# Performance work log

Measured on AMD Instinct MI355X. Metric: run time of the kernel, lower is better.

## Reference

```python
import jax, jax.numpy as jnp
import numpy as np

T_MAX = 0.5
LN_EPS = 1e-5
B, N, D = 256, 16384, 512
NNZ = N * 33  # ~ (2*top_k+1) nonzeros per row of the sparse Laplacian
DF = 4 * D
DT = 32  # time-embedding hidden size


def _layernorm(x, g, b):
    mu = jnp.mean(x, axis=-1, keepdims=True)
    var = jnp.mean((x - mu) ** 2, axis=-1, keepdims=True)
    return (x - mu) * jax.lax.rsqrt(var + LN_EPS) * g + b


def setup_inputs() -> dict:
    key = jax.random.key(0)
    ks = jax.random.split(key, 16)

    def lin_w(k, fan_out, fan_in):
        return jax.random.normal(k, (fan_out, fan_in), jnp.float32) * (1.0 / np.sqrt(fan_in))

    inp = {}
    inp["x0"] = jax.random.uniform(ks[0], (B, N), jnp.float32)
    inp["t"] = jax.random.uniform(ks[1], (B,), jnp.float32)
    inp["L_vals"] = jax.random.normal(ks[2], (NNZ,), jnp.float32) * 0.1
    inp["W_in"] = lin_w(ks[3], D, N)
    inp["b_in"] = jnp.zeros((D,), jnp.float32)
    inp["W_out"] = lin_w(ks[4], N, D)
    inp["b_out"] = jnp.zeros((N,), jnp.float32)
    inp["W_qkv"] = lin_w(ks[5], 3 * D, D)
    inp["b_qkv"] = jnp.zeros((3 * D,), jnp.float32)
    inp["W_o"] = lin_w(ks[6], D, D)
    inp["b_o"] = jnp.zeros((D,), jnp.float32)
    inp["g1"] = jnp.ones((D,), jnp.float32)
    inp["be1"] = jnp.zeros((D,), jnp.float32)
    inp["g2"] = jnp.ones((D,), jnp.float32)
    inp["be2"] = jnp.zeros((D,), jnp.float32)
    inp["W_f1"] = lin_w(ks[7], DF, D)
    inp["b_f1"] = jnp.zeros((DF,), jnp.float32)
    inp["W_f2"] = lin_w(ks[8], D, DF)
    inp["b_f2"] = jnp.zeros((D,), jnp.float32)
    inp["W_t1"] = lin_w(ks[9], DT, 1)
    inp["b_t1"] = jnp.zeros((DT,), jnp.float32)
    inp["W_t2"] = lin_w(ks[10], D, DT)
    inp["b_t2"] = jnp.zeros((D,), jnp.float32)
    inp["L_rows"] = jax.random.randint(ks[11], (NNZ,), 0, N, jnp.int32)
    inp["L_cols"] = jax.random.randint(ks[12], (NNZ,), 0, N, jnp.int32)
    return inp


def reference(x0, t, L_vals, W_in, b_in, W_out, b_out, W_qkv, b_qkv, W_o, b_o,
              g1, be1, g2, be2, W_f1, b_f1, W_f2, b_f2, W_t1, b_t1, W_t2, b_t2,
              L_rows, L_cols):
    n_items = x0.shape[1]
    d_model = W_in.shape[0]
    t_cont = t * T_MAX  # per-sample diffusion time (explicit input, not RNG)

    # Batched sparse Laplacian diffusion (replaces the per-row torch.sparse.mm loop):
    # (L @ x.T)[i, b] = sum_e L_vals[e] * x0[b, L_cols[e]] aggregated to row L_rows[e]
    contrib = x0[:, L_cols] * L_vals                                  # (B, NNZ)
    Lx = jax.ops.segment_sum(contrib.T, L_rows, num_segments=n_items)  # (N, B)
    x_t = x0 - t_cont[:, None] * Lx.T                                  # (B, N)

    # Denoiser (eval mode: dropout off)
    h = x_t @ W_in.T + b_in                                            # (B, D)
    t_norm = t_cont / T_MAX
    te = jax.nn.silu(t_norm[:, None] @ W_t1.T + b_t1) @ W_t2.T + b_t2  # (B, D)
    h = h + te

    # MultiheadAttention on a length-1 sequence: softmax over one key is exactly 1,
    # so attn_out = out_proj(V) with V = h @ W_v.T + b_v.
    qkv = h @ W_qkv.T + b_qkv                                          # (B, 3D)
    v = qkv[:, 2 * d_model:]
    attn_out = v @ W_o.T + b_o

    h = _layernorm(h + attn_out, g1, be1)
    ff = jax.nn.gelu(h @ W_f1.T + b_f1, approximate=False) @ W_f2.T + b_f2
    h = _layernorm(h + ff, g2, be2)

    pred = h @ W_out.T + b_out                                         # (B, N)
    return jnp.mean((pred - x0) ** 2)
```

## Files before the change

kernel.cpp:

```cpp
#include <hip/hip_runtime.h>
#include <math.h>

#define Bb   256
#define Nn   16384
#define Dd   512
#define NNZn 540672
#define DFf  2048
#define SLOT 128

typedef __bf16 bf16;
typedef __bf16 bf16x4 __attribute__((ext_vector_type(4)));
typedef __bf16 bf16x8 __attribute__((ext_vector_type(8)));
typedef float  f32x4  __attribute__((ext_vector_type(4)));

__device__ __forceinline__ void gload16(const void* g, void* l) {
  __builtin_amdgcn_global_load_lds(
      (const __attribute__((address_space(1))) unsigned int*)g,
      (__attribute__((address_space(3))) unsigned int*)l, 16, 0, 0);
}

__global__ __launch_bounds__(256) void k_cvt_all(
    const float* __restrict__ w_in, const float* __restrict__ w_out,
    const float* __restrict__ w_v, const float* __restrict__ w_o,
    const float* __restrict__ w_f1, const float* __restrict__ w_f2,
    bf16* __restrict__ o_in, bf16* __restrict__ o_out, bf16* __restrict__ o_v,
    bf16* __restrict__ o_o, bf16* __restrict__ o_f1, bf16* __restrict__ o_f2) {
  int v = blockIdx.x * 256 + threadIdx.x;
  const float* s; bf16* d; int base;
  if (v < 4194304) {
    if (v < 2097152) { s = w_in;  d = o_in;  base = 0; }
    else             { s = w_out; d = o_out; base = 2097152; }
  } else if (v < 4325376) {
    if (v < 4259840) { s = w_v;   d = o_v;   base = 4194304; }
    else             { s = w_o;   d = o_o;   base = 4259840; }
  } else {
    if (v < 4587520) { s = w_f1;  d = o_f1;  base = 4325376; }
    else             { s = w_f2;  d = o_f2;  base = 4587520; }
  }
  int idx = (v - base) * 4;
  float4 x = *(const float4*)(s + idx);
  bf16x4 o;
  o[0] = (bf16)x.x; o[1] = (bf16)x.y; o[2] = (bf16)x.z; o[3] = (bf16)x.w;
  *(bf16x4*)(d + idx) = o;
}

__global__ __launch_bounds__(256) void k_transpose(const float* __restrict__ x0,
                                                   bf16* __restrict__ x0T) {
  __shared__ float tile[64][65];
  int n0 = blockIdx.x * 64, b0 = blockIdx.y * 64;
  int tx = threadIdx.x & 63, ty = threadIdx.x >> 6;
#pragma unroll
  for (int i = 0; i < 16; i++) {
    int bl = ty * 16 + i;
    tile[bl][tx] = x0[(size_t)(b0 + bl) * Nn + n0 + tx];
  }
  __syncthreads();
#pragma unroll
  for (int i = 0; i < 16; i++) {
    int nl = ty * 16 + i;
    x0T[(size_t)(n0 + nl) * Bb + b0 + tx] = (bf16)tile[tx][nl];
  }
}

__global__ __launch_bounds__(256) void k_bucket(const int* __restrict__ rows,
                                                const int* __restrict__ cols,
                                                const float* __restrict__ vals,
                                                int* __restrict__ counts,
                                                int* __restrict__ cols_p,
                                                float* __restrict__ vals_p) {
  int i = blockIdx.x * 256 + threadIdx.x;
  int r = rows[i];
  int p = atomicAdd(&counts[r], 1);
  if (p < SLOT) {
    cols_p[(size_t)r * SLOT + p] = cols[i];
    vals_p[(size_t)r * SLOT + p] = vals[i];
  }
}

__global__ __launch_bounds__(256) void k_lx(const bf16x4* __restrict__ x0T4,
                                            const int* __restrict__ counts,
                                            const int* __restrict__ cols_p,
                                            const float* __restrict__ vals_p,
                                            bf16x4* __restrict__ Lx4) {
  int w = threadIdx.x >> 6, lane = threadIdx.x & 63;
  int r = blockIdx.x * 4 + w;
  __shared__ int   csm[4][64];
  __shared__ float vsm[4][64];
  int cnt = counts[r];
  const int*   cp = cols_p + (size_t)r * SLOT;
  const float* vp = vals_p + (size_t)r * SLOT;
  float a0 = 0.f, a1 = 0.f, a2 = 0.f, a3 = 0.f;
  float b0 = 0.f, b1 = 0.f, b2 = 0.f, b3 = 0.f;
  for (int base = 0; base < cnt; base += 64) {
    int m = cnt - base; if (m > 64) m = 64;
    if (lane < m) { csm[w][lane] = cp[base + lane]; vsm[w][lane] = vp[base + lane]; }
    int i = 0;
    for (; i + 1 < m; i += 2) {
      bf16x4 xv0 = x0T4[(size_t)csm[w][i]     * 64 + lane];
      bf16x4 xv1 = x0T4[(size_t)csm[w][i + 1] * 64 + lane];
      float v0 = vsm[w][i], v1 = vsm[w][i + 1];
      a0 += v0 * (float)xv0[0]; a1 += v0 * (float)xv0[1];
      a2 += v0 * (float)xv0[2]; a3 += v0 * (float)xv0[3];
      b0 += v1 * (float)xv1[0]; b1 += v1 * (float)xv1[1];
      b2 += v1 * (float)xv1[2]; b3 += v1 * (float)xv1[3];
    }
    if (i < m) {
      bf16x4 xv0 = x0T4[(size_t)csm[w][i] * 64 + lane];
      float v0 = vsm[w][i];
      a0 += v0 * (float)xv0[0]; a1 += v0 * (float)xv0[1];
      a2 += v0 * (float)xv0[2]; a3 += v0 * (float)xv0[3];
    }
  }
  bf16x4 o;
  o[0] = (bf16)(a0 + b0); o[1] = (bf16)(a1 + b1);
  o[2] = (bf16)(a2 + b2); o[3] = (bf16)(a3 + b3);
  Lx4[(size_t)r * 64 + lane] = o;
}

__global__ __launch_bounds__(256) void k_combine(const float* __restrict__ x0,
                                                 const bf16* __restrict__ Lx,
                                                 const float* __restrict__ t,
                                                 bf16* __restrict__ xt) {
  __shared__ float lxs[64][65];
  int n0 = blockIdx.x * 64, b0 = blockIdx.y * 64;
  int tx = threadIdx.x & 63, ty = threadIdx.x >> 6;
#pragma unroll
  for (int i = 0; i < 16; i++) {
    int nl = ty * 16 + i;
    lxs[nl][tx] = (float)Lx[(size_t)(n0 + nl) * Bb + b0 + tx];
  }
  __syncthreads();
#pragma unroll
  for (int i = 0; i < 16; i++) {
    int bl = ty * 16 + i;
    int b  = b0 + bl;
    float tc = t[b] * 0.5f;
    float v = x0[(size_t)b * Nn + n0 + tx] - tc * lxs[tx][bl];
    xt[(size_t)b * Nn + n0 + tx] = (bf16)v;
  }
}

template <int BM, int BN, int MODE, int ACT = 0>
__global__ __launch_bounds__(256) void gemm_tn(
    const bf16* __restrict__ A, const bf16* __restrict__ Bm,
    float* __restrict__ C, int N, int K, int kLen, int MN,
    const float* __restrict__ bias, const float* __restrict__ x0,
    float* __restrict__ lossOut) {
  constexpr int WM = BM / 2, WN = BN / 2, FM = WM / 16, FN = WN / 16;
  constexpr int PA = (BM * 64) / 4096, PB = (BN * 64) / 4096;
  __shared__ __align__(16) bf16 As[BM * 32];
  __shared__ __align__(16) bf16 Bs[BN * 32];
  const int tid = threadIdx.x;
  const int lane = tid & 63, w = tid >> 6;
  const int wm = w >> 1, wn = w & 1;
  const int mBase = blockIdx.x * BM, nBase = blockIdx.y * BN;
  const int k0 = blockIdx.z * kLen;

  f32x4 acc[FM][FN];
#pragma unroll
  for (int i = 0; i < FM; i++)
#pragma unroll
    for (int j = 0; j < FN; j++) acc[i][j] = {0.f, 0.f, 0.f, 0.f};

  for (int kk = 0; kk < kLen; kk += 32) {
    const int k = k0 + kk;
    __syncthreads();
#pragma unroll
    for (int p = 0; p < PA; p++) {
      int u = p * 256 + tid;
      gload16(A + (size_t)(mBase + (u >> 2)) * K + k + (u & 3) * 8,
              (char*)As + p * 4096 + w * 1024);
    }
#pragma unroll
    for (int p = 0; p < PB; p++) {
      int u = p * 256 + tid;
      gload16(Bm + (size_t)(nBase + (u >> 2)) * K + k + (u & 3) * 8,
              (char*)Bs + p * 4096 + w * 1024);
    }
    __syncthreads();
    bf16x8 af[FM], bfr[FN];
#pragma unroll
    for (int i = 0; i < FM; i++)
      af[i] = *(const bf16x8*)(As + (wm * WM + i * 16 + (lane & 15)) * 32 + (lane >> 4) * 8);
#pragma unroll
    for (int j = 0; j < FN; j++)
      bfr[j] = *(const bf16x8*)(Bs + (wn * WN + j * 16 + (lane & 15)) * 32 + (lane >> 4) * 8);
#pragma unroll
    for (int i = 0; i < FM; i++)
#pragma unroll
      for (int j = 0; j < FN; j++)
        acc[i][j] = __builtin_amdgcn_mfma_f32_16x16x32_bf16(af[i], bfr[j], acc[i][j], 0, 0, 0);
  }

  if constexpr (MODE == 0) {
    float* Cz = C + (size_t)blockIdx.z * MN;
#pragma unroll
    for (int i = 0; i < FM; i++)
#pragma unroll
      for (int j = 0; j < FN; j++) {
        int n  = nBase + wn * WN + j * 16 + (lane & 15);
        int mB = mBase + wm * WM + i * 16 + ((lane >> 4) << 2);
#pragma unroll
        for (int r = 0; r < 4; r++)
          Cz[(size_t)(mB + r) * N + n] = acc[i][j][r];
      }
  } else if constexpr (MODE == 1) {
    bf16* Cb = (bf16*)C;
#pragma unroll
    for (int i = 0; i < FM; i++)
#pragma unroll
      for (int j = 0; j < FN; j++) {
        int n  = nBase + wn * WN + j * 16 + (lane & 15);
        float bo = bias[n];
        int mB = mBase + wm * WM + i * 16 + ((lane >> 4) << 2);
#pragma unroll
        for (int r = 0; r < 4; r++) {
          float x = acc[i][j][r] + bo;
          if constexpr (ACT == 1)
            x = 0.5f * x * (1.f + erff(x * 0.70710678118654752f));
          Cb[(size_t)(mB + r) * N + n] = (bf16)x;
        }
      }
  } else {
    float lsum = 0.f;
#pragma unroll
    for (int i = 0; i < FM; i++)
#pragma unroll
      for (int j = 0; j < FN; j++) {
        int n  = nBase + wn * WN + j * 16 + (lane & 15);
        float bo = bias[n];
        int mB = mBase + wm * WM + i * 16 + ((lane >> 4) << 2);
#pragma unroll
        for (int r = 0; r < 4; r++) {
          float d = acc[i][j][r] + bo - x0[(size_t)(mB + r) * N + n];
          lsum += d * d;
        }
      }
    for (int off = 32; off > 0; off >>= 1) lsum += __shfl_down(lsum, off, 64);
    if (lane == 0) atomicAdd(lossOut, lsum);
  }
}

__global__ __launch_bounds__(512) void k_epi_h(const float* __restrict__ P,
                                               const float* __restrict__ t,
                                               const float* __restrict__ W_t1,
                                               const float* __restrict__ b_t1,
                                               const float* __restrict__ W_t2,
                                               const float* __restrict__ b_t2,
                                               const float* __restrict__ b_in,
                                               float* __restrict__ h_f32,
                                               bf16* __restrict__ h_b) {
  int b = blockIdx.x, d = threadIdx.x;
  __shared__ float s[32];
  if (d < 32) {
    float z = t[b] * W_t1[d] + b_t1[d];
    s[d] = z / (1.f + expf(-z));
  }
  __syncthreads();
  int i = b * Dd + d;
  float v = b_in[d] + b_t2[d];
#pragma unroll
  for (int sp = 0; sp < 32; sp++) v += P[sp * (Bb * Dd) + i];
#pragma unroll
  for (int j = 0; j < 32; j++) v += s[j] * W_t2[d * 32 + j];
  h_f32[i] = v;
  h_b[i] = (bf16)v;
}

template <int NS>
__global__ __launch_bounds__(512) void k_ln(const float* __restrict__ base,
                                            const float* __restrict__ add,
                                            const float* __restrict__ bias,
                                            const float* __restrict__ g,
                                            const float* __restrict__ be,
                                            float* __restrict__ out_f32,
                                            bf16* __restrict__ out_b) {
  int b = blockIdx.x, d = threadIdx.x;
  __shared__ float red[16];
  int i = b * Dd + d;
  float x = base[i] + bias[d];
#pragma unroll
  for (int sp = 0; sp < NS; sp++) x += add[sp * (Bb * Dd) + i];
  int w = d >> 6, lane = d & 63;
  float s = x;
  for (int off = 32; off > 0; off >>= 1) s += __shfl_down(s, off, 64);
  if (lane == 0) red[w] = s;
  __syncthreads();
  if (d == 0) {
    float tot = 0.f;
    for (int q = 0; q < 8; q++) tot += red[q];
    red[8] = tot * (1.f / 512.f);
  }
  __syncthreads();
  float mu = red[8];
  float c = x - mu;
  float s2 = c * c;
  for (int off = 32; off > 0; off >>= 1) s2 += __shfl_down(s2, off, 64);
  if (lane == 0) red[w] = s2;
  __syncthreads();
  if (d == 0) {
    float tot = 0.f;
    for (int q = 0; q < 8; q++) tot += red[q];
    red[8] = tot * (1.f / 512.f);
  }
  __syncthreads();
  float var = red[8];
  float y = c * rsqrtf(var + 1e-5f) * g[d] + be[d];
  if (out_f32) out_f32[i] = y;
  out_b[i] = (bf16)y;
}

__global__ void k_final(const float* __restrict__ loss, float* __restrict__ out) {
  if (threadIdx.x == 0 && blockIdx.x == 0)
    out[0] = loss[0] * (1.f / 4194304.f);
}

extern "C" void kernel_launch(void* const* d_in, const int* in_sizes, int n_in,
                              void* d_out, int out_size, void* d_ws, size_t ws_size,
                              hipStream_t stream) {
  const float* x0    = (const float*)d_in[0];
  const float* t     = (const float*)d_in[1];
  const float* Lv    = (const float*)d_in[2];
  const float* W_in  = (const float*)d_in[3];
  const float* b_in  = (const float*)d_in[4];
  const float* W_out = (const float*)d_in[5];
  const float* b_out = (const float*)d_in[6];
  const float* W_qkv = (const float*)d_in[7];
  const float* b_qkv = (const float*)d_in[8];
  const float* W_o   = (const float*)d_in[9];
  const float* b_o   = (const float*)d_in[10];
  const float* g1    = (const float*)d_in[11];
  const float* be1   = (const float*)d_in[12];
  const float* g2    = (const float*)d_in[13];
  const float* be2   = (const float*)d_in[14];
  const float* W_f1  = (const float*)d_in[15];
  const float* b_f1  = (const float*)d_in[16];
  const float* W_f2  = (const float*)d_in[17];
  const float* b_f2  = (const float*)d_in[18];
  const float* W_t1  = (const float*)d_in[19];
  const float* b_t1  = (const float*)d_in[20];
  const float* W_t2  = (const float*)d_in[21];
  const float* b_t2  = (const float*)d_in[22];
  const int* L_rows  = (const int*)d_in[23];
  const int* L_cols  = (const int*)d_in[24];

  size_t off = 0;
  char* ws = (char*)d_ws;
  auto carve = [&](size_t bytes) -> void* {
    void* p = ws + off;
    off += (bytes + 255) & ~(size_t)255;
    return p;
  };

  bf16* W_in_b   = (bf16*)carve((size_t)Dd * Nn * 2);
  bf16* W_out_b  = (bf16*)carve((size_t)Nn * Dd * 2);
  bf16* W_v_b    = (bf16*)carve((size_t)Dd * Dd * 2);
  bf16* W_o_b    = (bf16*)carve((size_t)Dd * Dd * 2);
  bf16* W_f1_b   = (bf16*)carve((size_t)DFf * Dd * 2);
  bf16* W_f2_b   = (bf16*)carve((size_t)Dd * DFf * 2);
  bf16* x0T_b    = (bf16*)carve((size_t)Nn * Bb * 2);
  bf16* Lx_b     = (bf16*)carve((size_t)Nn * Bb * 2);
  bf16* xt_b     = (bf16*)carve((size_t)Bb * Nn * 2);
  float* p_h     = (float*)carve((size_t)32 * Bb * Dd * 4);
  float* p_at    = (float*)carve((size_t)Bb * Dd * 4);
  float* p_f2    = (float*)carve((size_t)4 * Bb * Dd * 4);
  float* h_f32   = (float*)carve((size_t)Bb * Dd * 4);
  bf16* h_b      = (bf16*)carve((size_t)Bb * Dd * 2);
  bf16* v_b      = (bf16*)carve((size_t)Bb * Dd * 2);
  float* hln_f32 = (float*)carve((size_t)Bb * Dd * 4);
  bf16* hln_b    = (bf16*)carve((size_t)Bb * Dd * 2);
  bf16* f1_b     = (bf16*)carve((size_t)Bb * DFf * 2);
  bf16* h2_b     = (bf16*)carve((size_t)Bb * Dd * 2);
  int* counts    = (int*)carve((size_t)Nn * 4);
  float* lossw   = (float*)carve(256);
  int* cols_p    = (int*)carve((size_t)Nn * SLOT * 4);
  float* vals_p  = (float*)carve((size_t)Nn * SLOT * 4);
  (void)in_sizes; (void)n_in; (void)out_size; (void)ws_size;

  hipMemsetAsync(counts, 0, (size_t)Nn * 4 + 256, stream);

  k_cvt_all<<<18944, 256, 0, stream>>>(
      W_in, W_out, W_qkv + (size_t)2 * Dd * Dd, W_o, W_f1, W_f2,
      W_in_b, W_out_b, W_v_b, W_o_b, W_f1_b, W_f2_b);

  k_transpose<<<dim3(256, 4), 256, 0, stream>>>(x0, x0T_b);
  k_bucket<<<NNZn / 256, 256, 0, stream>>>(L_rows, L_cols, Lv, counts, cols_p, vals_p);
  k_lx<<<Nn / 4, 256, 0, stream>>>((const bf16x4*)x0T_b, counts, cols_p, vals_p,
                                   (bf16x4*)Lx_b);
  k_combine<<<dim3(256, 4), 256, 0, stream>>>(x0, Lx_b, t, xt_b);

  gemm_tn<128, 128, 0><<<dim3(2, 4, 32), 256, 0, stream>>>(
      xt_b, W_in_b, p_h, Dd, Nn, 512, Bb * Dd, nullptr, nullptr, nullptr);
  k_epi_h<<<Bb, 512, 0, stream>>>(p_h, t, W_t1, b_t1, W_t2, b_t2, b_in, h_f32, h_b);

  gemm_tn<64, 64, 1><<<dim3(4, 8, 1), 256, 0, stream>>>(
      h_b, W_v_b, (float*)v_b, Dd, Dd, 512, 0, b_qkv + 2 * Dd, nullptr, nullptr);

  gemm_tn<64, 64, 0><<<dim3(4, 8, 1), 256, 0, stream>>>(
      v_b, W_o_b, p_at, Dd, Dd, 512, 0, nullptr, nullptr, nullptr);
  k_ln<1><<<Bb, 512, 0, stream>>>(h_f32, p_at, b_o, g1, be1, hln_f32, hln_b);

  gemm_tn<64, 64, 1, 1><<<dim3(4, 32, 1), 256, 0, stream>>>(
      hln_b, W_f1_b, (float*)f1_b, DFf, Dd, 512, 0, b_f1, nullptr, nullptr);

  gemm_tn<64, 64, 0><<<dim3(4, 8, 4), 256, 0, stream>>>(
      f1_b, W_f2_b, p_f2, Dd, DFf, 512, Bb * Dd, nullptr, nullptr, nullptr);
  k_ln<4><<<Bb, 512, 0, stream>>>(hln_f32, p_f2, b_f2, g2, be2, nullptr, h2_b);

  gemm_tn<128, 128, 2><<<dim3(2, 128, 1), 256, 0, stream>>>(
      h2_b, W_out_b, nullptr, Nn, Dd, 512, 0, b_out, x0, lossw);
  k_final<<<1, 64, 0, stream>>>(lossw, (float*)d_out);
}
```

Before: 338.2 us.

## Fuse prep kernels, pack sparse entries, convert large weights inside GEMM loads

Merges the weight conversion, x0 transpose and COO bucketing into one launch. It drops the separate fp32-to-bf16 passes for the two large N×D weights (W_in, W_out); their GEMMs now read fp32 B tiles and convert them while storing to shared memory. Sparse column and value pairs are stored together as int2, so k_lx does one load per entry instead of two. This removes a large conversion write and read plus two launches. The trade is that those GEMMs move twice the B bytes and use synchronous register-staged loads instead of direct global-to-LDS loads.

New measurement: 329.6 us. -2.5%, faster.

```diff
diff --git a/kernel.cpp b/kernel.cpp
--- a/kernel.cpp
+++ b/kernel.cpp
@@ -8,6 +8,10 @@
 #define DFf  2048
 #define SLOT 128
 
+#define CVT_BLKS 2560
+#define TR_BLKS  1024
+#define BK_BLKS  2112
+
 typedef __bf16 bf16;
 typedef __bf16 bf16x4 __attribute__((ext_vector_type(4)));
 typedef __bf16 bf16x8 __attribute__((ext_vector_type(8)));
@@ -19,94 +23,85 @@
       (__attribute__((address_space(3))) unsigned int*)l, 16, 0, 0);
 }
 
-__global__ __launch_bounds__(256) void k_cvt_all(
-    const float* __restrict__ w_in, const float* __restrict__ w_out,
+__global__ __launch_bounds__(256) void k_prep(
     const float* __restrict__ w_v, const float* __restrict__ w_o,
     const float* __restrict__ w_f1, const float* __restrict__ w_f2,
-    bf16* __restrict__ o_in, bf16* __restrict__ o_out, bf16* __restrict__ o_v,
-    bf16* __restrict__ o_o, bf16* __restrict__ o_f1, bf16* __restrict__ o_f2) {
-  int v = blockIdx.x * 256 + threadIdx.x;
-  const float* s; bf16* d; int base;
-  if (v < 4194304) {
-    if (v < 2097152) { s = w_in;  d = o_in;  base = 0; }
-    else             { s = w_out; d = o_out; base = 2097152; }
-  } else if (v < 4325376) {
-    if (v < 4259840) { s = w_v;   d = o_v;   base = 4194304; }
-    else             { s = w_o;   d = o_o;   base = 4259840; }
+    bf16* __restrict__ o_v, bf16* __restrict__ o_o,
+    bf16* __restrict__ o_f1, bf16* __restrict__ o_f2,
+    const float* __restrict__ x0, bf16* __restrict__ x0T,
+    const int* __restrict__ rows, const int* __restrict__ cols,
+    const float* __restrict__ vals,
+    int* __restrict__ counts, int2* __restrict__ ents) {
+  __shared__ float tile[64][65];
+  int blk = blockIdx.x;
+  if (blk < CVT_BLKS) {
+    int v = blk * 256 + threadIdx.x;
+    const float* s; bf16* d; int base;
+    if (v < 131072) {
+      if (v < 65536) { s = w_v;  d = o_v;  base = 0; }
+      else           { s = w_o;  d = o_o;  base = 65536; }
+    } else {
+      if (v < 393216) { s = w_f1; d = o_f1; base = 131072; }
+      else            { s = w_f2; d = o_f2; base = 393216; }
+    }
+    int idx = (v - base) * 4;
+    float4 x = *(const float4*)(s + idx);
+    bf16x4 o;
+    o[0] = (bf16)x.x; o[1] = (bf16)x.y; o[2] = (bf16)x.z; o[3] = (bf16)x.w;
+    *(bf16x4*)(d + idx) = o;
+  } else if (blk < CVT_BLKS + TR_BLKS) {
+    int bx = blk - CVT_BLKS;
+    int n0 = (bx & 255) * 64, b0 = (bx >> 8) * 64;
+    int tx = threadIdx.x & 63, ty = threadIdx.x >> 6;
+#pragma unroll
+    for (int i = 0; i < 16; i++) {
+      int bl = ty * 16 + i;
+      tile[bl][tx] = x0[(size_t)(b0 + bl) * Nn + n0 + tx];
+    }
+    __syncthreads();
+#pragma unroll
+    for (int i = 0; i < 16; i++) {
+      int nl = ty * 16 + i;
+      x0T[(size_t)(n0 + nl) * Bb + b0 + tx] = (bf16)tile[tx][nl];
+    }
   } else {
-    if (v < 4587520) { s = w_f1;  d = o_f1;  base = 4325376; }
-    else             { s = w_f2;  d = o_f2;  base = 4587520; }
-  }
-  int idx = (v - base) * 4;
-  float4 x = *(const float4*)(s + idx);
-  bf16x4 o;
-  o[0] = (bf16)x.x; o[1] = (bf16)x.y; o[2] = (bf16)x.z; o[3] = (bf16)x.w;
-  *(bf16x4*)(d + idx) = o;
-}
-
-__global__ __launch_bounds__(256) void k_transpose(const float* __restrict__ x0,
-                                                   bf16* __restrict__ x0T) {
-  __shared__ float tile[64][65];
-  int n0 = blockIdx.x * 64, b0 = blockIdx.y * 64;
-  int tx = threadIdx.x & 63, ty = threadIdx.x >> 6;
-#pragma unroll
-  for (int i = 0; i < 16; i++) {
-    int bl = ty * 16 + i;
-    tile[bl][tx] = x0[(size_t)(b0 + bl) * Nn + n0 + tx];
-  }
-  __syncthreads();
-#pragma unroll
-  for (int i = 0; i < 16; i++) {
-    int nl = ty * 16 + i;
-    x0T[(size_t)(n0 + nl) * Bb + b0 + tx] = (bf16)tile[tx][nl];
-  }
-}
-
-__global__ __launch_bounds__(256) void k_bucket(const int* __restrict__ rows,
-                                                const int* __restrict__ cols,
-                                                const float* __restrict__ vals,
-                                                int* __restrict__ counts,
-                                                int* __restrict__ cols_p,
-                                                float* __restrict__ vals_p) {
-  int i = blockIdx.x * 256 + threadIdx.x;
-  int r = rows[i];
-  int p = atomicAdd(&counts[r], 1);
-  if (p < SLOT) {
-    cols_p[(size_t)r * SLOT + p] = cols[i];
-    vals_p[(size_t)r * SLOT + p] = vals[i];
+    int i = (blk - CVT_BLKS - TR_BLKS) * 256 + threadIdx.x;
+    int r = rows[i];
+    int p = atomicAdd(&counts[r], 1);
+    if (p < SLOT)
+      ents[(size_t)r * SLOT + p] = make_int2(cols[i], __float_as_int(vals[i]));
   }
 }
 
 __global__ __launch_bounds__(256) void k_lx(const bf16x4* __restrict__ x0T4,
                                             const int* __restrict__ counts,
-                                            const int* __restrict__ cols_p,
-                                            const float* __restrict__ vals_p,
+                                            const int2* __restrict__ ents,
                                             bf16x4* __restrict__ Lx4) {
   int w = threadIdx.x >> 6, lane = threadIdx.x & 63;
   int r = blockIdx.x * 4 + w;
-  __shared__ int   csm[4][64];
-  __shared__ float vsm[4][64];
+  __shared__ int2 esm[4][64];
   int cnt = counts[r];
-  const int*   cp = cols_p + (size_t)r * SLOT;
-  const float* vp = vals_p + (size_t)r * SLOT;
+  const int2* ep = ents + (size_t)r * SLOT;
   float a0 = 0.f, a1 = 0.f, a2 = 0.f, a3 = 0.f;
   float b0 = 0.f, b1 = 0.f, b2 = 0.f, b3 = 0.f;
   for (int base = 0; base < cnt; base += 64) {
     int m = cnt - base; if (m > 64) m = 64;
-    if (lane < m) { csm[w][lane] = cp[base + lane]; vsm[w][lane] = vp[base + lane]; }
+    if (lane < m) esm[w][lane] = ep[base + lane];
     int i = 0;
     for (; i + 1 < m; i += 2) {
-      bf16x4 xv0 = x0T4[(size_t)csm[w][i]     * 64 + lane];
-      bf16x4 xv1 = x0T4[(size_t)csm[w][i + 1] * 64 + lane];
-      float v0 = vsm[w][i], v1 = vsm[w][i + 1];
+      int2 e0 = esm[w][i], e1 = esm[w][i + 1];
+      bf16x4 xv0 = x0T4[(size_t)e0.x * 64 + lane];
+      bf16x4 xv1 = x0T4[(size_t)e1.x * 64 + lane];
+      float v0 = __int_as_float(e0.y), v1 = __int_as_float(e1.y);
       a0 += v0 * (float)xv0[0]; a1 += v0 * (float)xv0[1];
       a2 += v0 * (float)xv0[2]; a3 += v0 * (float)xv0[3];
       b0 += v1 * (float)xv1[0]; b1 += v1 * (float)xv1[1];
       b2 += v1 * (float)xv1[2]; b3 += v1 * (float)xv1[3];
     }
     if (i < m) {
-      bf16x4 xv0 = x0T4[(size_t)csm[w][i] * 64 + lane];
-      float v0 = vsm[w][i];
+      int2 e0 = esm[w][i];
+      bf16x4 xv0 = x0T4[(size_t)e0.x * 64 + lane];
+      float v0 = __int_as_float(e0.y);
       a0 += v0 * (float)xv0[0]; a1 += v0 * (float)xv0[1];
       a2 += v0 * (float)xv0[2]; a3 += v0 * (float)xv0[3];
     }
@@ -140,9 +135,9 @@
   }
 }
 
-template <int BM, int BN, int MODE, int ACT = 0>
+template <int BM, int BN, int MODE, int ACT = 0, int BF32 = 0>
 __global__ __launch_bounds__(256) void gemm_tn(
-    const bf16* __restrict__ A, const bf16* __restrict__ Bm,
+    const bf16* __restrict__ A, const void* __restrict__ Bmv,
     float* __restrict__ C, int N, int K, int kLen, int MN,
     const float* __restrict__ bias, const float* __restrict__ x0,
     float* __restrict__ lossOut) {
@@ -171,11 +166,25 @@
       gload16(A + (size_t)(mBase + (u >> 2)) * K + k + (u & 3) * 8,
               (char*)As + p * 4096 + w * 1024);
     }
-#pragma unroll
-    for (int p = 0; p < PB; p++) {
-      int u = p * 256 + tid;
-      gload16(Bm + (size_t)(nBase + (u >> 2)) * K + k + (u & 3) * 8,
-              (char*)Bs + p * 4096 + w * 1024);
+    if constexpr (BF32) {
+      const float* Bf = (const float*)Bmv;
+#pragma unroll
+      for (int p = 0; p < BN * 32 / 1024; p++) {
+        int u = p * 256 + tid;
+        int row = u >> 3, sub = u & 7;
+        float4 x = *(const float4*)(Bf + (size_t)(nBase + row) * K + k + sub * 4);
+        bf16x4 o;
+        o[0] = (bf16)x.x; o[1] = (bf16)x.y; o[2] = (bf16)x.z; o[3] = (bf16)x.w;
+        *(bf16x4*)(Bs + row * 32 + sub * 4) = o;
+      }
+    } else {
+      const bf16* Bm = (const bf16*)Bmv;
+#pragma unroll
+      for (int p = 0; p < PB; p++) {
+        int u = p * 256 + tid;
+        gload16(Bm + (size_t)(nBase + (u >> 2)) * K + k + (u & 3) * 8,
+                (char*)Bs + p * 4096 + w * 1024);
+      }
     }
     __syncthreads();
     bf16x8 af[FM], bfr[FN];
@@ -352,8 +361,6 @@
     return p;
   };
 
-  bf16* W_in_b   = (bf16*)carve((size_t)Dd * Nn * 2);
-  bf16* W_out_b  = (bf16*)carve((size_t)Nn * Dd * 2);
   bf16* W_v_b    = (bf16*)carve((size_t)Dd * Dd * 2);
   bf16* W_o_b    = (bf16*)carve((size_t)Dd * Dd * 2);
   bf16* W_f1_b   = (bf16*)carve((size_t)DFf * Dd * 2);
@@ -373,24 +380,22 @@
   bf16* h2_b     = (bf16*)carve((size_t)Bb * Dd * 2);
   int* counts    = (int*)carve((size_t)Nn * 4);
   float* lossw   = (float*)carve(256);
-  int* cols_p    = (int*)carve((size_t)Nn * SLOT * 4);
-  float* vals_p  = (float*)carve((size_t)Nn * SLOT * 4);
-  (void)in_sizes; (void)n_in; (void)out_size; (void)ws_size;
+  int2* ents     = (int2*)carve((size_t)Nn * SLOT * 8);
+  (void)in_sizes; (void)n_in; (void)out_size; (void)ws_size; (void)Lv;
 
   hipMemsetAsync(counts, 0, (size_t)Nn * 4 + 256, stream);
 
-  k_cvt_all<<<18944, 256, 0, stream>>>(
-      W_in, W_out, W_qkv + (size_t)2 * Dd * Dd, W_o, W_f1, W_f2,
-      W_in_b, W_out_b, W_v_b, W_o_b, W_f1_b, W_f2_b);
-
-  k_transpose<<<dim3(256, 4), 256, 0, stream>>>(x0, x0T_b);
-  k_bucket<<<NNZn / 256, 256, 0, stream>>>(L_rows, L_cols, Lv, counts, cols_p, vals_p);
-  k_lx<<<Nn / 4, 256, 0, stream>>>((const bf16x4*)x0T_b, counts, cols_p, vals_p,
+  k_prep<<<CVT_BLKS + TR_BLKS + BK_BLKS, 256, 0, stream>>>(
+      W_qkv + (size_t)2 * Dd * Dd, W_o, W_f1, W_f2,
+      W_v_b, W_o_b, W_f1_b, W_f2_b,
+      x0, x0T_b, L_rows, L_cols, Lv, counts, ents);
+
+  k_lx<<<Nn / 4, 256, 0, stream>>>((const bf16x4*)x0T_b, counts, ents,
                                    (bf16x4*)Lx_b);
   k_combine<<<dim3(256, 4), 256, 0, stream>>>(x0, Lx_b, t, xt_b);
 
-  gemm_tn<128, 128, 0><<<dim3(2, 4, 32), 256, 0, stream>>>(
-      xt_b, W_in_b, p_h, Dd, Nn, 512, Bb * Dd, nullptr, nullptr, nullptr);
+  gemm_tn<128, 128, 0, 0, 1><<<dim3(2, 4, 32), 256, 0, stream>>>(
+      xt_b, W_in, p_h, Dd, Nn, 512, Bb * Dd, nullptr, nullptr, nullptr);
   k_epi_h<<<Bb, 512, 0, stream>>>(p_h, t, W_t1, b_t1, W_t2, b_t2, b_in, h_f32, h_b);
 
   gemm_tn<64, 64, 1><<<dim3(4, 8, 1), 256, 0, stream>>>(
@@ -407,7 +412,7 @@
       f1_b, W_f2_b, p_f2, Dd, DFf, 512, Bb * Dd, nullptr, nullptr, nullptr);
   k_ln<4><<<Bb, 512, 0, stream>>>(hln_f32, p_f2, b_f2, g2, be2, nullptr, h2_b);
 
-  gemm_tn<128, 128, 2><<<dim3(2, 128, 1), 256, 0, stream>>>(
-      h2_b, W_out_b, nullptr, Nn, Dd, 512, 0, b_out, x0, lossw);
+  gemm_tn<128, 128, 2, 0, 1><<<dim3(2, 128, 1), 256, 0, stream>>>(
+      h2_b, W_out, nullptr, Nn, Dd, 512, 0, b_out, x0, lossw);
   k_final<<<1, 64, 0, stream>>>(lossw, (float*)d_out);
 }
```
